# Performance work log

Hardware: AMD Instinct MI355X
Metric: run time of the kernel (lower is better)

Reference implementation:

```python
import jax, jax.numpy as jnp
import numpy as np

N_NODES = 100000
N_EDGES = 1600000
D_IN = 128
D_HID = 256
D_OUT = 128


def setup_inputs() -> dict:
    key = jax.random.key(0)
    ks = jax.random.split(key, 8)
    x = jax.random.normal(ks[0], (N_NODES, D_IN), dtype=jnp.float32)
    edge_vals = jax.random.uniform(ks[1], (N_EDGES,), dtype=jnp.float32)
    # MLP params, scaled for numerical stability (fan-in style)
    W1 = jax.random.normal(ks[2], (D_IN, D_HID), dtype=jnp.float32) / np.sqrt(D_IN)
    b1 = jnp.zeros((D_HID,), dtype=jnp.float32)
    W2 = jax.random.normal(ks[3], (D_HID, D_OUT), dtype=jnp.float32) / np.sqrt(D_HID)
    b2 = jnp.zeros((D_OUT,), dtype=jnp.float32)
    eps = jnp.zeros((1,), dtype=jnp.float32)
    edge_src = jax.random.randint(ks[4], (N_EDGES,), 0, N_NODES, dtype=jnp.int32)
    edge_dst = jax.random.randint(ks[5], (N_EDGES,), 0, N_NODES, dtype=jnp.int32)
    return {
        "x": x, "edge_vals": edge_vals,
        "W1": W1, "b1": b1, "W2": W2, "b2": b2,
        "eps": eps, "edge_src": edge_src, "edge_dst": edge_dst,
    }


def reference(x, edge_vals, W1, b1, W2, b2, eps, edge_src, edge_dst):
    # Sparse SpMM: AX = A @ x with A in COO (dst <- val * x[src]).
    # dropout_rate=0 -> identity; single support matrix.
    gathered = edge_vals[:, None] * x[edge_src]            # [E, D_in]
    AX = jax.ops.segment_sum(gathered, edge_dst, num_segments=x.shape[0])  # [N, D_in]
    # GIN self-loop combine
    h = AX + (1.0 + eps) * x                                # [N, D_in]
    # MLP_for_GIN (2 layers): Linear -> ReLU -> Linear
    h = jax.nn.relu(h @ W1 + b1)                            # [N, D_hid]
    out = h @ W2 + b2                                       # [N, D_out]
    # act_func=None -> no final activation
    return out
```

## Files before the change

kernel.cpp:

```cpp
#include <hip/hip_runtime.h>
#include <hip/hip_bf16.h>

typedef __attribute__((ext_vector_type(8))) __bf16 bf16x8;
typedef __attribute__((ext_vector_type(4))) float f32x4;

#define NN 100000
#define NE 1600000
#define NBK 6250
#define SUP 49
#define CAPA 36864
#define EPB 2048
#define NBA 782
#define NSLC 16
#define CAPB 384

__device__ __forceinline__ float bflo(unsigned w) { return __uint_as_float(w << 16); }
__device__ __forceinline__ float bfhi(unsigned w) { return __uint_as_float(w & 0xffff0000u); }

__global__ __launch_bounds__(512) void front_kernel(const float* __restrict__ W1,
                                                    const float* __restrict__ W2,
                                                    __bf16* __restrict__ W1T,
                                                    __bf16* __restrict__ W2T,
                                                    const float4* __restrict__ x4,
                                                    uint2* __restrict__ xb,
                                                    const int* __restrict__ esrc,
                                                    const int* __restrict__ edst,
                                                    const float* __restrict__ ev,
                                                    int* __restrict__ supercnt,
                                                    int2* __restrict__ psup) {
    __shared__ int scnt[SUP], sbase[SUP], scur[SUP];
    const int b = blockIdx.x, t = threadIdx.x;

    if (b < 64) {
        int tid = b * 512 + t;
        int k1 = tid >> 8, n1 = tid & 255;
        W1T[n1 * 128 + k1] = (__bf16)W1[tid];
        int k2 = tid >> 7, n2 = tid & 127;
        W2T[n2 * 256 + k2] = (__bf16)W2[tid];
    }
    for (int i = b * 512 + t; i < NN * 32; i += NBA * 512) {
        float4 v = x4[i];
        __bf16 b0 = (__bf16)v.x, b1 = (__bf16)v.y, b2 = (__bf16)v.z, b3 = (__bf16)v.w;
        uint2 o;
        o.x = (unsigned)*(unsigned short*)&b0 | ((unsigned)*(unsigned short*)&b1 << 16);
        o.y = (unsigned)*(unsigned short*)&b2 | ((unsigned)*(unsigned short*)&b3 << 16);
        xb[i] = o;
    }
    const int lo = b * EPB;
    const int hi = (lo + EPB < NE) ? lo + EPB : NE;
    if (t < SUP) scnt[t] = 0;
    __syncthreads();
    for (int e = lo + t; e < hi; e += 512)
        atomicAdd(&scnt[edst[e] >> 11], 1);
    __syncthreads();
    if (t < SUP) {
        int c = scnt[t];
        sbase[t] = c ? atomicAdd(&supercnt[t], c) : 0;
        scur[t] = 0;
    }
    __syncthreads();
    for (int e = lo + t; e < hi; e += 512) {
        int d = edst[e];
        int s = esrc[e];
        float v = ev[e];
        int sp = d >> 11;
        int off = sbase[sp] + atomicAdd(&scur[sp], 1);
        if (off < CAPA) {
            int2 p; p.x = (s << 11) | (d & 0x7FF); p.y = __float_as_int(v);
            psup[(size_t)sp * CAPA + off] = p;
        }
    }
}

__global__ __launch_bounds__(512) void refine_kernel(const int2* __restrict__ psup,
                                                     const int* __restrict__ supercnt,
                                                     int* __restrict__ bktcnt,
                                                     int2* __restrict__ pairs2) {
    __shared__ int lcnt[128], lbase[128], lcur[128];
    const int s = blockIdx.x / NSLC, sl = blockIdx.x % NSLC, t = threadIdx.x;
    int cnt = supercnt[s]; if (cnt > CAPA) cnt = CAPA;
    const int per = (cnt + NSLC - 1) / NSLC;
    const int beg = sl * per;
    const int end = (beg + per < cnt) ? beg + per : cnt;
    const int2* seg = psup + (size_t)s * CAPA;

    if (t < 128) lcnt[t] = 0;
    __syncthreads();
    for (int i = beg + t; i < end; i += 512)
        atomicAdd(&lcnt[(seg[i].x >> 4) & 127], 1);
    __syncthreads();
    if (t < 128) {
        int c = lcnt[t];
        lbase[t] = c ? atomicAdd(&bktcnt[(s << 7) + t], c) : 0;
        lcur[t] = 0;
    }
    __syncthreads();
    for (int i = beg + t; i < end; i += 512) {
        int2 p = seg[i];
        int sub = (p.x >> 4) & 127;
        int off = lbase[sub] + atomicAdd(&lcur[sub], 1);
        if (off < CAPB)
            pairs2[(size_t)((s << 7) + sub) * CAPB + off] = p;
    }
}

__global__ __launch_bounds__(1024) void sort_gather_kernel(const unsigned* __restrict__ xb,
                                                           const int* __restrict__ bktcnt,
                                                           const int2* __restrict__ pairs2,
                                                           const float* __restrict__ eps,
                                                           uint2* __restrict__ AXb) {
    __shared__ int2 raw[CAPB];
    __shared__ int2 srt[CAPB];
    __shared__ int rcnt[16], rofs[16], rcur[16];

    const int t = threadIdx.x;
    const int b = blockIdx.x;
    const int wave = t >> 6, lane = t & 63;
    const unsigned hw = lane >> 5, l32 = lane & 31u;
    const char* xbase = (const char*)xb + l32 * 8;

    int m = bktcnt[b]; if (m > CAPB) m = CAPB;
    const int2* seg = pairs2 + (size_t)b * CAPB;

    if (t < 16) rcnt[t] = 0;
    __syncthreads();
    for (int i = t; i < m; i += 1024) {
        int2 p = seg[i];
        raw[i] = p;
        atomicAdd(&rcnt[p.x & 15], 1);
    }
    __syncthreads();
    if (t == 0) {
        int run = 0;
#pragma unroll
        for (int r = 0; r < 16; ++r) { rofs[r] = run; rcur[r] = run; run += rcnt[r]; }
    }
    __syncthreads();
    for (int i = t; i < m; i += 1024) {
        int2 p = raw[i];
        int pos = atomicAdd(&rcur[p.x & 15], 1);
        int2 q; q.x = (p.x >> 3) & 0xFFFFFF00;
        q.y = p.y;
        srt[pos] = q;
    }
    __syncthreads();

    float a0 = 0.f, a1 = 0.f, a2 = 0.f, a3 = 0.f;
    {
        const int je = rofs[wave] + rcnt[wave];
        int j = rofs[wave] + (int)hw;
        for (; j + 6 < je; j += 8) {
            int2 e0 = srt[j], e1 = srt[j + 2], e2 = srt[j + 4], e3 = srt[j + 6];
            uint2 w0 = *(const uint2*)(xbase + e0.x);
            uint2 w1 = *(const uint2*)(xbase + e1.x);
            uint2 w2 = *(const uint2*)(xbase + e2.x);
            uint2 w3 = *(const uint2*)(xbase + e3.x);
            float v0 = __int_as_float(e0.y), v1 = __int_as_float(e1.y);
            float v2 = __int_as_float(e2.y), v3 = __int_as_float(e3.y);
            a0 = fmaf(v0, bflo(w0.x), a0); a1 = fmaf(v0, bfhi(w0.x), a1);
            a2 = fmaf(v0, bflo(w0.y), a2); a3 = fmaf(v0, bfhi(w0.y), a3);
            a0 = fmaf(v1, bflo(w1.x), a0); a1 = fmaf(v1, bfhi(w1.x), a1);
            a2 = fmaf(v1, bflo(w1.y), a2); a3 = fmaf(v1, bfhi(w1.y), a3);
            a0 = fmaf(v2, bflo(w2.x), a0); a1 = fmaf(v2, bfhi(w2.x), a1);
            a2 = fmaf(v2, bflo(w2.y), a2); a3 = fmaf(v2, bfhi(w2.y), a3);
            a0 = fmaf(v3, bflo(w3.x), a0); a1 = fmaf(v3, bfhi(w3.x), a1);
            a2 = fmaf(v3, bflo(w3.y), a2); a3 = fmaf(v3, bfhi(w3.y), a3);
        }
        for (; j < je; j += 2) {
            int2 e0 = srt[j];
            uint2 w0 = *(const uint2*)(xbase + e0.x);
            float v0 = __int_as_float(e0.y);
            a0 = fmaf(v0, bflo(w0.x), a0); a1 = fmaf(v0, bfhi(w0.x), a1);
            a2 = fmaf(v0, bflo(w0.y), a2); a3 = fmaf(v0, bfhi(w0.y), a3);
        }
    }

    a0 += __shfl_xor(a0, 32); a1 += __shfl_xor(a1, 32);
    a2 += __shfl_xor(a2, 32); a3 += __shfl_xor(a3, 32);
    if (hw == 0) {
        const int n = b * 16 + wave;
        uint2 ws = *(const uint2*)(xbase + (size_t)n * 256);
        float sc = 1.0f + eps[0];
        a0 = fmaf(sc, bflo(ws.x), a0); a1 = fmaf(sc, bfhi(ws.x), a1);
        a2 = fmaf(sc, bflo(ws.y), a2); a3 = fmaf(sc, bfhi(ws.y), a3);
        __bf16 b0 = (__bf16)a0, b1 = (__bf16)a1, b2 = (__bf16)a2, b3 = (__bf16)a3;
        uint2 o;
        o.x = (unsigned)*(unsigned short*)&b0 | ((unsigned)*(unsigned short*)&b1 << 16);
        o.y = (unsigned)*(unsigned short*)&b2 | ((unsigned)*(unsigned short*)&b3 << 16);
        AXb[(size_t)n * 32 + l32] = o;
    }
}

__global__ void convert_w_kernel(const float* __restrict__ W1, const float* __restrict__ W2,
                                 __bf16* __restrict__ W1T, __bf16* __restrict__ W2T) {
    int tid = blockIdx.x * 256 + threadIdx.x;
    if (tid < 128 * 256) {
        int k1 = tid >> 8, n1 = tid & 255;
        W1T[n1 * 128 + k1] = (__bf16)W1[tid];
        int k2 = tid >> 7, n2 = tid & 127;
        W2T[n2 * 256 + k2] = (__bf16)W2[tid];
    }
}

__global__ void init_ax_kernel(const float4* __restrict__ x, float4* __restrict__ AX,
                               const float* __restrict__ eps, int n4) {
    int i = blockIdx.x * blockDim.x + threadIdx.x;
    if (i >= n4) return;
    float s = 1.0f + eps[0];
    float4 v = x[i];
    v.x *= s; v.y *= s; v.z *= s; v.w *= s;
    AX[i] = v;
}

__global__ void scatter_kernel(const float2* __restrict__ x2, const float* __restrict__ ev,
                               const int* __restrict__ esrc, const int* __restrict__ edst,
                               float* AX) {
    unsigned gid = blockIdx.x * 256u + threadIdx.x;
    unsigned e = gid >> 6;
    unsigned lane = gid & 63u;
    if (e >= NE) return;
    float v = ev[e];
    int s = esrc[e], d = edst[e];
    float2 xv = x2[(size_t)s * 64 + lane];
    float* dstp = AX + (size_t)d * 128 + lane * 2;
    atomicAdd(dstp,     v * xv.x);
    atomicAdd(dstp + 1, v * xv.y);
}

template <typename AT>
__global__ __launch_bounds__(256) void mlp_kernel(const AT* A,
                                                  const __bf16* __restrict__ W1T,
                                                  const __bf16* __restrict__ W2T,
                                                  const float* __restrict__ b1,
                                                  const float* __restrict__ b2,
                                                  float* out) {
    __shared__ __bf16 Hl[64][264];

    const int wave = threadIdx.x >> 6;
    const int lane = threadIdx.x & 63;
    const int l15  = lane & 15;
    const int lhi  = lane >> 4;
    const int rowbase = blockIdx.x * 64;

    f32x4 acc1[4][4] = {};
#pragma unroll
    for (int ks = 0; ks < 4; ++ks) {
        const int k0 = ks * 32 + lhi * 8;
        bf16x8 am[4], bn[4];
#pragma unroll
        for (int mt = 0; mt < 4; ++mt) {
            int row = rowbase + mt * 16 + l15;
            if (row >= NN) row = NN - 1;
            if constexpr (__is_same(AT, __bf16)) {
                am[mt] = *(const bf16x8*)(A + (size_t)row * 128 + k0);
            } else {
                const float4* ap = (const float4*)(A + (size_t)row * 128 + k0);
                float4 f0 = ap[0], f1 = ap[1];
                bf16x8 a;
                a[0]=(__bf16)f0.x; a[1]=(__bf16)f0.y; a[2]=(__bf16)f0.z; a[3]=(__bf16)f0.w;
                a[4]=(__bf16)f1.x; a[5]=(__bf16)f1.y; a[6]=(__bf16)f1.z; a[7]=(__bf16)f1.w;
                am[mt] = a;
            }
        }
#pragma unroll
        for (int nt = 0; nt < 4; ++nt) {
            int n = wave * 64 + nt * 16 + l15;
            bn[nt] = *(const bf16x8*)(W1T + (size_t)n * 128 + k0);
        }
#pragma unroll
        for (int mt = 0; mt < 4; ++mt)
#pragma unroll
            for (int nt = 0; nt < 4; ++nt)
                acc1[mt][nt] = __builtin_amdgcn_mfma_f32_16x16x32_bf16(am[mt], bn[nt], acc1[mt][nt], 0, 0, 0);
    }

#pragma unroll
    for (int nt = 0; nt < 4; ++nt) {
        int n = wave * 64 + nt * 16 + l15;
        float bias = b1[n];
#pragma unroll
        for (int mt = 0; mt < 4; ++mt)
#pragma unroll
            for (int r = 0; r < 4; ++r) {
                float h = acc1[mt][nt][r] + bias;
                Hl[mt * 16 + lhi * 4 + r][n] = (__bf16)fmaxf(h, 0.0f);
            }
    }
    __syncthreads();

    f32x4 acc2[4][2] = {};
#pragma unroll
    for (int ks = 0; ks < 8; ++ks) {
        const int k0 = ks * 32 + lhi * 8;
        bf16x8 ha[4], wb[2];
#pragma unroll
        for (int mt = 0; mt < 4; ++mt)
            ha[mt] = *(const bf16x8*)(&Hl[mt * 16 + l15][k0]);
#pragma unroll
        for (int nt = 0; nt < 2; ++nt) {
            int n = wave * 32 + nt * 16 + l15;
            wb[nt] = *(const bf16x8*)(W2T + (size_t)n * 256 + k0);
        }
#pragma unroll
        for (int mt = 0; mt < 4; ++mt)
#pragma unroll
            for (int nt = 0; nt < 2; ++nt)
                acc2[mt][nt] = __builtin_amdgcn_mfma_f32_16x16x32_bf16(ha[mt], wb[nt], acc2[mt][nt], 0, 0, 0);
    }

#pragma unroll
    for (int nt = 0; nt < 2; ++nt) {
        int n = wave * 32 + nt * 16 + l15;
        float bias = b2[n];
#pragma unroll
        for (int mt = 0; mt < 4; ++mt)
#pragma unroll
            for (int r = 0; r < 4; ++r) {
                int row = rowbase + mt * 16 + lhi * 4 + r;
                if (row < NN) out[(size_t)row * 128 + n] = acc2[mt][nt][r] + bias;
            }
    }
}

extern "C" void kernel_launch(void* const* d_in, const int* in_sizes, int n_in,
                              void* d_out, int out_size, void* d_ws, size_t ws_size,
                              hipStream_t stream) {
    const float* x    = (const float*)d_in[0];
    const float* ev   = (const float*)d_in[1];
    const float* W1   = (const float*)d_in[2];
    const float* b1   = (const float*)d_in[3];
    const float* W2   = (const float*)d_in[4];
    const float* b2   = (const float*)d_in[5];
    const float* eps  = (const float*)d_in[6];
    const int*   esrc = (const int*)d_in[7];
    const int*   edst = (const int*)d_in[8];
    float* out = (float*)d_out;

    char* ws = (char*)d_ws;
    size_t off = 0;
    auto alloc = [&](size_t bytes) { void* p = ws + off; off += (bytes + 511) & ~size_t(511); return p; };

    __bf16* W1T   = (__bf16*)alloc(128 * 256 * sizeof(__bf16));
    __bf16* W2T   = (__bf16*)alloc(128 * 256 * sizeof(__bf16));
    int* cnts     = (int*)  alloc((size_t)(SUP + NBK) * sizeof(int));
    int2* psup    = (int2*) alloc((size_t)SUP * CAPA * sizeof(int2));
    int2* pairs2  = (int2*) alloc((size_t)NBK * CAPB * sizeof(int2));
    unsigned* xb  = (unsigned*)alloc((size_t)NN * 64 * sizeof(unsigned));
    unsigned* AXb = (unsigned*)alloc((size_t)NN * 64 * sizeof(unsigned));
    bool csr_ok = (off <= ws_size);

    if (csr_ok) {
        int* supercnt = cnts;
        int* bktcnt   = cnts + SUP;
        hipMemsetAsync(cnts, 0, (size_t)(SUP + NBK) * sizeof(int), stream);
        front_kernel<<<NBA, 512, 0, stream>>>(W1, W2, W1T, W2T, (const float4*)x,
                                              (uint2*)xb, esrc, edst, ev, supercnt, psup);
        refine_kernel<<<SUP * NSLC, 512, 0, stream>>>(psup, supercnt, bktcnt, pairs2);
        sort_gather_kernel<<<NBK, 1024, 0, stream>>>(xb, bktcnt, pairs2, eps, (uint2*)AXb);
        int nblk = (NN + 63) / 64;
        mlp_kernel<__bf16><<<nblk, 256, 0, stream>>>((const __bf16*)AXb, W1T, W2T, b1, b2, out);
    } else {
        __bf16* W1Tf = (__bf16*)ws;
        __bf16* W2Tf = W1Tf + 128 * 256;
        convert_w_kernel<<<128, 256, 0, stream>>>(W1, W2, W1Tf, W2Tf);
        int n4 = NN * 128 / 4;
        init_ax_kernel<<<(n4 + 255) / 256, 256, 0, stream>>>((const float4*)x, (float4*)out, eps, n4);
        scatter_kernel<<<(NE * 64u) / 256u, 256, 0, stream>>>((const float2*)x, ev, esrc, edst, out);
        int nblk = (NN + 63) / 64;
        mlp_kernel<float><<<nblk, 256, 0, stream>>>(out, W1Tf, W2Tf, b1, b2, out);
    }
}
```

Before: 178.0 us.

## Fuse sorted gather with two-layer MLP in one kernel via LDS tile

Replaces the separate sort_gather and mlp kernels with a single gather_mlp_kernel. Each 1024-thread block processes four 16-node buckets, writes the bf16 aggregated rows into an LDS tile, then runs both MFMA GEMM layers from LDS and writes the final output. This removes the AXb global round trip and one kernel launch. In exchange the grid is four times smaller, the gather phases run serially within each block with extra barriers, and each block's MLP uses 16 waves over only 64 rows, which may lower occupancy and overlap.

```diff
diff --git a/kernel.cpp b/kernel.cpp
--- a/kernel.cpp
+++ b/kernel.cpp
@@ -7,12 +7,14 @@
 #define NN 100000
 #define NE 1600000
 #define NBK 6250
+#define NBG 1563
 #define SUP 49
 #define CAPA 36864
 #define EPB 2048
 #define NBA 782
 #define NSLC 16
 #define CAPB 384
+#define AST 136
 
 __device__ __forceinline__ float bflo(unsigned w) { return __uint_as_float(w << 16); }
 __device__ __forceinline__ float bfhi(unsigned w) { return __uint_as_float(w & 0xffff0000u); }
@@ -104,90 +106,162 @@
     }
 }
 
-__global__ __launch_bounds__(1024) void sort_gather_kernel(const unsigned* __restrict__ xb,
-                                                           const int* __restrict__ bktcnt,
-                                                           const int2* __restrict__ pairs2,
-                                                           const float* __restrict__ eps,
-                                                           uint2* __restrict__ AXb) {
-    __shared__ int2 raw[CAPB];
-    __shared__ int2 srt[CAPB];
+__global__ __launch_bounds__(1024) void gather_mlp_kernel(const unsigned* __restrict__ xb,
+                                                          const int* __restrict__ bktcnt,
+                                                          const int2* __restrict__ pairs2,
+                                                          const float* __restrict__ eps,
+                                                          const __bf16* __restrict__ W1T,
+                                                          const __bf16* __restrict__ W2T,
+                                                          const float* __restrict__ b1,
+                                                          const float* __restrict__ b2,
+                                                          float* __restrict__ out) {
+    __shared__ __attribute__((aligned(16))) char smem[17408 + 33792];
+    __bf16* At  = (__bf16*)smem;
+    char*   X   = smem + 17408;
+    int2*   raw = (int2*)X;
+    int2*   srt = (int2*)(X + 3072);
+    __bf16* Hl  = (__bf16*)X;
     __shared__ int rcnt[16], rofs[16], rcur[16];
 
     const int t = threadIdx.x;
-    const int b = blockIdx.x;
+    const int B = blockIdx.x;
     const int wave = t >> 6, lane = t & 63;
     const unsigned hw = lane >> 5, l32 = lane & 31u;
     const char* xbase = (const char*)xb + l32 * 8;
-
-    int m = bktcnt[b]; if (m > CAPB) m = CAPB;
-    const int2* seg = pairs2 + (size_t)b * CAPB;
-
-    if (t < 16) rcnt[t] = 0;
-    __syncthreads();
-    for (int i = t; i < m; i += 1024) {
-        int2 p = seg[i];
-        raw[i] = p;
-        atomicAdd(&rcnt[p.x & 15], 1);
-    }
-    __syncthreads();
-    if (t == 0) {
-        int run = 0;
-#pragma unroll
-        for (int r = 0; r < 16; ++r) { rofs[r] = run; rcur[r] = run; run += rcnt[r]; }
-    }
-    __syncthreads();
-    for (int i = t; i < m; i += 1024) {
-        int2 p = raw[i];
-        int pos = atomicAdd(&rcur[p.x & 15], 1);
-        int2 q; q.x = (p.x >> 3) & 0xFFFFFF00;
-        q.y = p.y;
-        srt[pos] = q;
-    }
-    __syncthreads();
-
-    float a0 = 0.f, a1 = 0.f, a2 = 0.f, a3 = 0.f;
+    const float sc = 1.0f + eps[0];
+
+    for (int c = 0; c < 4; ++c) {
+        const int bk = B * 4 + c;
+        int m = (bk < NBK) ? bktcnt[bk] : 0;
+        if (m > CAPB) m = CAPB;
+        const int2* seg = pairs2 + (size_t)bk * CAPB;
+
+        __syncthreads();
+        if (t < 16) rcnt[t] = 0;
+        __syncthreads();
+        for (int i = t; i < m; i += 1024) {
+            int2 p = seg[i];
+            raw[i] = p;
+            atomicAdd(&rcnt[p.x & 15], 1);
+        }
+        __syncthreads();
+        if (t == 0) {
+            int run = 0;
+#pragma unroll
+            for (int r = 0; r < 16; ++r) { rofs[r] = run; rcur[r] = run; run += rcnt[r]; }
+        }
+        __syncthreads();
+        for (int i = t; i < m; i += 1024) {
+            int2 p = raw[i];
+            int pos = atomicAdd(&rcur[p.x & 15], 1);
+            int2 q; q.x = (p.x >> 3) & 0xFFFFFF00;
+            q.y = p.y;
+            srt[pos] = q;
+        }
+        __syncthreads();
+
+        float a0 = 0.f, a1 = 0.f, a2 = 0.f, a3 = 0.f;
+        {
+            const int je = rofs[wave] + rcnt[wave];
+            int j = rofs[wave] + (int)hw;
+            for (; j + 6 < je; j += 8) {
+                int2 e0 = srt[j], e1 = srt[j + 2], e2 = srt[j + 4], e3 = srt[j + 6];
+                uint2 w0 = *(const uint2*)(xbase + e0.x);
+                uint2 w1 = *(const uint2*)(xbase + e1.x);
+                uint2 w2 = *(const uint2*)(xbase + e2.x);
+                uint2 w3 = *(const uint2*)(xbase + e3.x);
+                float v0 = __int_as_float(e0.y), v1 = __int_as_float(e1.y);
+                float v2 = __int_as_float(e2.y), v3 = __int_as_float(e3.y);
+                a0 = fmaf(v0, bflo(w0.x), a0); a1 = fmaf(v0, bfhi(w0.x), a1);
+                a2 = fmaf(v0, bflo(w0.y), a2); a3 = fmaf(v0, bfhi(w0.y), a3);
+                a0 = fmaf(v1, bflo(w1.x), a0); a1 = fmaf(v1, bfhi(w1.x), a1);
+                a2 = fmaf(v1, bflo(w1.y), a2); a3 = fmaf(v1, bfhi(w1.y), a3);
+                a0 = fmaf(v2, bflo(w2.x), a0); a1 = fmaf(v2, bfhi(w2.x), a1);
+                a2 = fmaf(v2, bflo(w2.y), a2); a3 = fmaf(v2, bfhi(w2.y), a3);
+                a0 = fmaf(v3, bflo(w3.x), a0); a1 = fmaf(v3, bfhi(w3.x), a1);
+                a2 = fmaf(v3, bflo(w3.y), a2); a3 = fmaf(v3, bfhi(w3.y), a3);
+            }
+            for (; j < je; j += 2) {
+                int2 e0 = srt[j];
+                uint2 w0 = *(const uint2*)(xbase + e0.x);
+                float v0 = __int_as_float(e0.y);
+                a0 = fmaf(v0, bflo(w0.x), a0); a1 = fmaf(v0, bfhi(w0.x), a1);
+                a2 = fmaf(v0, bflo(w0.y), a2); a3 = fmaf(v0, bfhi(w0.y), a3);
+            }
+        }
+        a0 += __shfl_xor(a0, 32); a1 += __shfl_xor(a1, 32);
+        a2 += __shfl_xor(a2, 32); a3 += __shfl_xor(a3, 32);
+        if (hw == 0) {
+            const int n = bk * 16 + wave;
+            unsigned p0 = 0, p1 = 0;
+            if (n < NN) {
+                uint2 ws = *(const uint2*)(xbase + (size_t)n * 256);
+                a0 = fmaf(sc, bflo(ws.x), a0); a1 = fmaf(sc, bfhi(ws.x), a1);
+                a2 = fmaf(sc, bflo(ws.y), a2); a3 = fmaf(sc, bfhi(ws.y), a3);
+                __bf16 c0 = (__bf16)a0, c1 = (__bf16)a1, c2 = (__bf16)a2, c3 = (__bf16)a3;
+                p0 = (unsigned)*(unsigned short*)&c0 | ((unsigned)*(unsigned short*)&c1 << 16);
+                p1 = (unsigned)*(unsigned short*)&c2 | ((unsigned)*(unsigned short*)&c3 << 16);
+            }
+            const int r = c * 16 + wave;
+            uint2 o; o.x = p0; o.y = p1;
+            *(uint2*)((char*)At + (size_t)r * (AST * 2) + l32 * 8) = o;
+        }
+    }
+    __syncthreads();
+
+    const int l15 = lane & 15, lhi = lane >> 4;
+
     {
-        const int je = rofs[wave] + rcnt[wave];
-        int j = rofs[wave] + (int)hw;
-        for (; j + 6 < je; j += 8) {
-            int2 e0 = srt[j], e1 = srt[j + 2], e2 = srt[j + 4], e3 = srt[j + 6];
-            uint2 w0 = *(const uint2*)(xbase + e0.x);
-            uint2 w1 = *(const uint2*)(xbase + e1.x);
-            uint2 w2 = *(const uint2*)(xbase + e2.x);
-            uint2 w3 = *(const uint2*)(xbase + e3.x);
-            float v0 = __int_as_float(e0.y), v1 = __int_as_float(e1.y);
-            float v2 = __int_as_float(e2.y), v3 = __int_as_float(e3.y);
-            a0 = fmaf(v0, bflo(w0.x), a0); a1 = fmaf(v0, bfhi(w0.x), a1);
-            a2 = fmaf(v0, bflo(w0.y), a2); a3 = fmaf(v0, bfhi(w0.y), a3);
-            a0 = fmaf(v1, bflo(w1.x), a0); a1 = fmaf(v1, bfhi(w1.x), a1);
-            a2 = fmaf(v1, bflo(w1.y), a2); a3 = fmaf(v1, bfhi(w1.y), a3);
-            a0 = fmaf(v2, bflo(w2.x), a0); a1 = fmaf(v2, bfhi(w2.x), a1);
-            a2 = fmaf(v2, bflo(w2.y), a2); a3 = fmaf(v2, bfhi(w2.y), a3);
-            a0 = fmaf(v3, bflo(w3.x), a0); a1 = fmaf(v3, bfhi(w3.x), a1);
-            a2 = fmaf(v3, bflo(w3.y), a2); a3 = fmaf(v3, bfhi(w3.y), a3);
-        }
-        for (; j < je; j += 2) {
-            int2 e0 = srt[j];
-            uint2 w0 = *(const uint2*)(xbase + e0.x);
-            float v0 = __int_as_float(e0.y);
-            a0 = fmaf(v0, bflo(w0.x), a0); a1 = fmaf(v0, bfhi(w0.x), a1);
-            a2 = fmaf(v0, bflo(w0.y), a2); a3 = fmaf(v0, bfhi(w0.y), a3);
-        }
-    }
-
-    a0 += __shfl_xor(a0, 32); a1 += __shfl_xor(a1, 32);
-    a2 += __shfl_xor(a2, 32); a3 += __shfl_xor(a3, 32);
-    if (hw == 0) {
-        const int n = b * 16 + wave;
-        uint2 ws = *(const uint2*)(xbase + (size_t)n * 256);
-        float sc = 1.0f + eps[0];
-        a0 = fmaf(sc, bflo(ws.x), a0); a1 = fmaf(sc, bfhi(ws.x), a1);
-        a2 = fmaf(sc, bflo(ws.y), a2); a3 = fmaf(sc, bfhi(ws.y), a3);
-        __bf16 b0 = (__bf16)a0, b1 = (__bf16)a1, b2 = (__bf16)a2, b3 = (__bf16)a3;
-        uint2 o;
-        o.x = (unsigned)*(unsigned short*)&b0 | ((unsigned)*(unsigned short*)&b1 << 16);
-        o.y = (unsigned)*(unsigned short*)&b2 | ((unsigned)*(unsigned short*)&b3 << 16);
-        AXb[(size_t)n * 32 + l32] = o;
+        f32x4 acc1[4] = {};
+        const int n = wave * 16 + l15;
+        const __bf16* w1p = W1T + (size_t)n * 128;
+#pragma unroll
+        for (int ks = 0; ks < 4; ++ks) {
+            const int k0 = ks * 32 + lhi * 8;
+            bf16x8 bn = *(const bf16x8*)(w1p + k0);
+#pragma unroll
+            for (int mt = 0; mt < 4; ++mt) {
+                bf16x8 am = *(const bf16x8*)(At + (size_t)(mt * 16 + l15) * AST + k0);
+                acc1[mt] = __builtin_amdgcn_mfma_f32_16x16x32_bf16(am, bn, acc1[mt], 0, 0, 0);
+            }
+        }
+        float bias = b1[n];
+#pragma unroll
+        for (int mt = 0; mt < 4; ++mt)
+#pragma unroll
+            for (int r = 0; r < 4; ++r) {
+                float h = acc1[mt][r] + bias;
+                Hl[(size_t)(mt * 16 + lhi * 4 + r) * 264 + n] = (__bf16)fmaxf(h, 0.0f);
+            }
+    }
+    __syncthreads();
+
+    {
+        f32x4 acc2[2] = {};
+#pragma unroll
+        for (int ks = 0; ks < 8; ++ks) {
+            const int k0 = ks * 32 + lhi * 8;
+#pragma unroll
+            for (int a = 0; a < 2; ++a) {
+                const int idx = wave * 2 + a;
+                const int mt = idx >> 3, nt = idx & 7;
+                bf16x8 ha = *(const bf16x8*)(Hl + (size_t)(mt * 16 + l15) * 264 + k0);
+                bf16x8 wb = *(const bf16x8*)(W2T + (size_t)(nt * 16 + l15) * 256 + k0);
+                acc2[a] = __builtin_amdgcn_mfma_f32_16x16x32_bf16(ha, wb, acc2[a], 0, 0, 0);
+            }
+        }
+#pragma unroll
+        for (int a = 0; a < 2; ++a) {
+            const int idx = wave * 2 + a;
+            const int mt = idx >> 3, nt = idx & 7;
+            const int col = nt * 16 + l15;
+            float bias = b2[col];
+#pragma unroll
+            for (int r = 0; r < 4; ++r) {
+                int row = B * 64 + mt * 16 + lhi * 4 + r;
+                if (row < NN) out[(size_t)row * 128 + col] = acc2[a][r] + bias;
+            }
+        }
     }
 }
 
@@ -227,15 +301,13 @@
     atomicAdd(dstp + 1, v * xv.y);
 }
 
-template <typename AT>
-__global__ __launch_bounds__(256) void mlp_kernel(const AT* A,
+__global__ __launch_bounds__(256) void mlp_kernel(const float* A,
                                                   const __bf16* __restrict__ W1T,
                                                   const __bf16* __restrict__ W2T,
                                                   const float* __restrict__ b1,
                                                   const float* __restrict__ b2,
                                                   float* out) {
     __shared__ __bf16 Hl[64][264];
-
     const int wave = threadIdx.x >> 6;
     const int lane = threadIdx.x & 63;
     const int l15  = lane & 15;
@@ -251,16 +323,12 @@
         for (int mt = 0; mt < 4; ++mt) {
             int row = rowbase + mt * 16 + l15;
             if (row >= NN) row = NN - 1;
-            if constexpr (__is_same(AT, __bf16)) {
-                am[mt] = *(const bf16x8*)(A + (size_t)row * 128 + k0);
-            } else {
-                const float4* ap = (const float4*)(A + (size_t)row * 128 + k0);
-                float4 f0 = ap[0], f1 = ap[1];
-                bf16x8 a;
-                a[0]=(__bf16)f0.x; a[1]=(__bf16)f0.y; a[2]=(__bf16)f0.z; a[3]=(__bf16)f0.w;
-                a[4]=(__bf16)f1.x; a[5]=(__bf16)f1.y; a[6]=(__bf16)f1.z; a[7]=(__bf16)f1.w;
-                am[mt] = a;
-            }
+            const float4* ap = (const float4*)(A + (size_t)row * 128 + k0);
+            float4 f0 = ap[0], f1 = ap[1];
+            bf16x8 a;
+            a[0]=(__bf16)f0.x; a[1]=(__bf16)f0.y; a[2]=(__bf16)f0.z; a[3]=(__bf16)f0.w;
+            a[4]=(__bf16)f1.x; a[5]=(__bf16)f1.y; a[6]=(__bf16)f1.z; a[7]=(__bf16)f1.w;
+            am[mt] = a;
         }
 #pragma unroll
         for (int nt = 0; nt < 4; ++nt) {
@@ -273,7 +341,6 @@
             for (int nt = 0; nt < 4; ++nt)
                 acc1[mt][nt] = __builtin_amdgcn_mfma_f32_16x16x32_bf16(am[mt], bn[nt], acc1[mt][nt], 0, 0, 0);
     }
-
 #pragma unroll
     for (int nt = 0; nt < 4; ++nt) {
         int n = wave * 64 + nt * 16 + l15;
@@ -307,7 +374,6 @@
             for (int nt = 0; nt < 2; ++nt)
                 acc2[mt][nt] = __builtin_amdgcn_mfma_f32_16x16x32_bf16(ha[mt], wb[nt], acc2[mt][nt], 0, 0, 0);
     }
-
 #pragma unroll
     for (int nt = 0; nt < 2; ++nt) {
         int n = wave * 32 + nt * 16 + l15;
@@ -346,7 +412,6 @@
     int2* psup    = (int2*) alloc((size_t)SUP * CAPA * sizeof(int2));
     int2* pairs2  = (int2*) alloc((size_t)NBK * CAPB * sizeof(int2));
     unsigned* xb  = (unsigned*)alloc((size_t)NN * 64 * sizeof(unsigned));
-    unsigned* AXb = (unsigned*)alloc((size_t)NN * 64 * sizeof(unsigned));
     bool csr_ok = (off <= ws_size);
 
     if (csr_ok) {
@@ -356,9 +421,8 @@
         front_kernel<<<NBA, 512, 0, stream>>>(W1, W2, W1T, W2T, (const float4*)x,
                                               (uint2*)xb, esrc, edst, ev, supercnt, psup);
         refine_kernel<<<SUP * NSLC, 512, 0, stream>>>(psup, supercnt, bktcnt, pairs2);
-        sort_gather_kernel<<<NBK, 1024, 0, stream>>>(xb, bktcnt, pairs2, eps, (uint2*)AXb);
-        int nblk = (NN + 63) / 64;
-        mlp_kernel<__bf16><<<nblk, 256, 0, stream>>>((const __bf16*)AXb, W1T, W2T, b1, b2, out);
+        gather_mlp_kernel<<<NBG, 1024, 0, stream>>>(xb, bktcnt, pairs2, eps,
+                                                    W1T, W2T, b1, b2, out);
     } else {
         __bf16* W1Tf = (__bf16*)ws;
         __bf16* W2Tf = W1Tf + 128 * 256;
@@ -367,6 +431,6 @@
         init_ax_kernel<<<(n4 + 255) / 256, 256, 0, stream>>>((const float4*)x, (float4*)out, eps, n4);
         scatter_kernel<<<(NE * 64u) / 256u, 256, 0, stream>>>((const float2*)x, ev, esrc, edst, out);
         int nblk = (NN + 63) / 64;
-        mlp_kernel<float><<<nblk, 256, 0, stream>>>(out, W1Tf, W2Tf, b1, b2, out);
-    }
-}
+        mlp_kernel<<<nblk, 256, 0, stream>>>(out, W1Tf, W2Tf, b1, b2, out);
+    }
+}
```

Measured after the change: 202.0 us. +13.5%, slower.
